# Optimization experiments

Measured on AMD Instinct MI355X. Metric: run time of the kernel, lower is better.

## Reference

```python
import jax, jax.numpy as jnp
import numpy as np

N_HEAD, D_MODEL, D_K, D_V = 8, 128, 16, 16
EPS = 1e-5


def entmax15(x):
    # 1.5-entmax along last axis (Peters & Martins 2019, exact sort-based algo)
    x = x * 0.5
    x = x - jnp.max(x, axis=-1, keepdims=True)
    xs = jnp.flip(jnp.sort(x, axis=-1), axis=-1)  # descending
    K = x.shape[-1]
    rho = jnp.arange(1, K + 1, dtype=x.dtype)
    mean = jnp.cumsum(xs, axis=-1) / rho
    mean_sq = jnp.cumsum(xs * xs, axis=-1) / rho
    delta = (1.0 - rho * (mean_sq - mean * mean)) / rho
    tau = mean - jnp.sqrt(jnp.clip(delta, 0.0))
    support = jnp.sum(tau <= xs, axis=-1, keepdims=True)  # support size k*
    tau_star = jnp.take_along_axis(tau, support - 1, axis=-1)
    p = jnp.clip(x - tau_star, 0.0)
    return p * p


def layer_norm(x, gamma, beta):
    mu = jnp.mean(x, axis=-1, keepdims=True)
    var = jnp.mean((x - mu) ** 2, axis=-1, keepdims=True)
    return gamma * (x - mu) * jax.lax.rsqrt(var + EPS) + beta


def setup_inputs() -> dict:
    key = jax.random.key(0)
    ks = jax.random.split(key, 24)
    B, Lq, Lk, D = 4, 1024, 2048, D_MODEL
    s = 0.05
    f = jax.random.normal
    return {
        "q": f(ks[0], (B, Lq, D), jnp.float32),
        "k": f(ks[1], (B, Lk, D), jnp.float32),
        "v": f(ks[2], (B, Lk, D), jnp.float32),
        "v_2": f(ks[3], (B, Lq, D), jnp.float32),
        "W_Q": f(ks[4], (D, N_HEAD * D_K)) * s, "b_Q": f(ks[5], (N_HEAD * D_K,)) * s,
        "W_K": f(ks[6], (D, N_HEAD * D_K)) * s, "b_K": f(ks[7], (N_HEAD * D_K,)) * s,
        "W_V": f(ks[8], (D, N_HEAD * D_V)) * s, "b_V": f(ks[9], (N_HEAD * D_V,)) * s,
        "W_V2": f(ks[10], (D, N_HEAD * D_V)) * s, "b_V2": f(ks[11], (N_HEAD * D_V,)) * s,
        "W_O": f(ks[12], (N_HEAD * D_V, D)) * s, "b_O": f(ks[13], (D,)) * s,
        "W_O2": f(ks[14], (N_HEAD * D_V, D)) * s, "b_O2": f(ks[15], (D,)) * s,
        "W_R": f(ks[16], (D, D)) * s,
        "W_R2": f(ks[17], (D, D)) * s,
        "gamma": jnp.ones((D,), jnp.float32),
        "beta": jnp.zeros((D,), jnp.float32),
    }


def reference(q, k, v, v_2, W_Q, b_Q, W_K, b_K, W_V, b_V, W_V2, b_V2,
              W_O, b_O, W_O2, b_O2, W_R, W_R2, gamma, beta):
    B, Lq, _ = q.shape
    Lk = k.shape[1]
    Q = (q @ W_Q + b_Q).reshape(B, Lq, N_HEAD, D_K)
    Kh = (k @ W_K + b_K).reshape(B, Lk, N_HEAD, D_K)
    V = (v @ W_V + b_V).reshape(B, Lk, N_HEAD, D_V)
    V2 = (v_2 @ W_V2 + b_V2).reshape(B, Lq, N_HEAD, D_V)
    # scores: [B, H, Lq, Lk]
    scores = jnp.einsum('bqhd,bkhd->bhqk', Q, Kh) / np.float32(np.sqrt(D_K))
    A = entmax15(scores)                              # normalize over Lk
    A2 = entmax15(jnp.swapaxes(scores, -2, -1))       # normalize over Lq
    out = jnp.einsum('bhqk,bkhd->bqhd', A, V).reshape(B, Lq, N_HEAD * D_V)
    out2 = jnp.einsum('bhkq,bqhd->bkhd', A2, V2).reshape(B, Lk, N_HEAD * D_V)
    # dropout is identity in eval mode; both branches use the SAME layer_norm params (as in source)
    out = jax.nn.relu(layer_norm(out @ W_O + b_O + q @ W_R, gamma, beta))
    out2 = jax.nn.relu(layer_norm(out2 @ W_O2 + b_O2 + k @ W_R2, gamma, beta))
    return (out, out2, A, A2)
```

## Files before the change

kernel.cpp:

```cpp
#include <hip/hip_runtime.h>

__device__ __forceinline__ float dpp_scan_add(float x)
{
  x += __int_as_float(__builtin_amdgcn_update_dpp(0, __float_as_int(x), 0x111, 0xf, 0xf, true));
  x += __int_as_float(__builtin_amdgcn_update_dpp(0, __float_as_int(x), 0x112, 0xf, 0xf, true));
  x += __int_as_float(__builtin_amdgcn_update_dpp(0, __float_as_int(x), 0x114, 0xf, 0xf, true));
  x += __int_as_float(__builtin_amdgcn_update_dpp(0, __float_as_int(x), 0x118, 0xf, 0xf, true));
  x += __int_as_float(__builtin_amdgcn_update_dpp(0, __float_as_int(x), 0x142, 0xa, 0xf, true));
  x += __int_as_float(__builtin_amdgcn_update_dpp(0, __float_as_int(x), 0x143, 0xc, 0xf, true));
  return x;
}
__device__ __forceinline__ int dpp_scan_add_i(int x)
{
  x += __builtin_amdgcn_update_dpp(0, x, 0x111, 0xf, 0xf, true);
  x += __builtin_amdgcn_update_dpp(0, x, 0x112, 0xf, 0xf, true);
  x += __builtin_amdgcn_update_dpp(0, x, 0x114, 0xf, 0xf, true);
  x += __builtin_amdgcn_update_dpp(0, x, 0x118, 0xf, 0xf, true);
  x += __builtin_amdgcn_update_dpp(0, x, 0x142, 0xa, 0xf, true);
  x += __builtin_amdgcn_update_dpp(0, x, 0x143, 0xc, 0xf, true);
  return x;
}
__device__ __forceinline__ float wave_bcast63(float x)
{
  return __int_as_float(__builtin_amdgcn_readlane(__float_as_int(x), 63));
}
__device__ __forceinline__ float wave_sum(float x)
{
  return wave_bcast63(dpp_scan_add(x));
}
__device__ __forceinline__ float wave_max(float x)
{
  x = fmaxf(x, __int_as_float(__builtin_amdgcn_update_dpp(__float_as_int(x), __float_as_int(x), 0x111, 0xf, 0xf, false)));
  x = fmaxf(x, __int_as_float(__builtin_amdgcn_update_dpp(__float_as_int(x), __float_as_int(x), 0x112, 0xf, 0xf, false)));
  x = fmaxf(x, __int_as_float(__builtin_amdgcn_update_dpp(__float_as_int(x), __float_as_int(x), 0x114, 0xf, 0xf, false)));
  x = fmaxf(x, __int_as_float(__builtin_amdgcn_update_dpp(__float_as_int(x), __float_as_int(x), 0x118, 0xf, 0xf, false)));
  x = fmaxf(x, __int_as_float(__builtin_amdgcn_update_dpp(__float_as_int(x), __float_as_int(x), 0x142, 0xa, 0xf, false)));
  x = fmaxf(x, __int_as_float(__builtin_amdgcn_update_dpp(__float_as_int(x), __float_as_int(x), 0x143, 0xc, 0xf, false)));
  return wave_bcast63(x);
}

__global__ __launch_bounds__(128) void proj_all_kernel(
    const float* __restrict__ q, const float* __restrict__ k,
    const float* __restrict__ v, const float* __restrict__ v2,
    const float* __restrict__ W_Q, const float* __restrict__ b_Q,
    const float* __restrict__ W_K, const float* __restrict__ b_K,
    const float* __restrict__ W_V, const float* __restrict__ b_V,
    const float* __restrict__ W_V2, const float* __restrict__ b_V2,
    float* __restrict__ Qp, float* __restrict__ Kp,
    float* __restrict__ Vp, float* __restrict__ V2p)
{
  __shared__ float xs[4][128];
  int blk = blockIdx.x;
  const float *X, *W, *B; float* Y; int L, chunked, rb;
  if (blk < 1024)      { X = q;  W = W_Q;  B = b_Q;  Y = Qp;  L = 1024; chunked = 1; rb = blk; }
  else if (blk < 3072) { X = k;  W = W_K;  B = b_K;  Y = Kp;  L = 2048; chunked = 1; rb = blk - 1024; }
  else if (blk < 5120) { X = v;  W = W_V;  B = b_V;  Y = Vp;  L = 2048; chunked = 0; rb = blk - 3072; }
  else                 { X = v2; W = W_V2; B = b_V2; Y = V2p; L = 1024; chunked = 0; rb = blk - 5120; }
  rb *= 4;
  int c = threadIdx.x;
#pragma unroll
  for (int i = 0; i < 4; ++i)
    xs[i][c] = X[(size_t)(rb + i) * 128 + c];
  __syncthreads();
  float b = B[c];
  float a0 = b, a1 = b, a2 = b, a3 = b;
#pragma unroll 8
  for (int d = 0; d < 128; ++d) {
    float w = W[d * 128 + c];
    a0 = fmaf(xs[0][d], w, a0);
    a1 = fmaf(xs[1][d], w, a1);
    a2 = fmaf(xs[2][d], w, a2);
    a3 = fmaf(xs[3][d], w, a3);
  }
  int h = c >> 4, dd = c & 15;
  float av[4] = { a0, a1, a2, a3 };
#pragma unroll
  for (int i = 0; i < 4; ++i) {
    int row = rb + i;
    int bb = row / L;
    int l  = row - bb * L;
    if (chunked)
      Y[(((size_t)(bb * 8 + h) * 4 + (dd >> 2)) * L + l) * 4 + (dd & 3)] = av[i];
    else
      Y[((size_t)(bb * 8 + h) * L + l) * 16 + dd] = av[i];
  }
}

static __device__ __forceinline__ float hstep(float f, float s1, float cnt)
{
  float arg = fmaf(-cnt, f, s1 * s1);
  return (arg > 0.f) ? f / (s1 + sqrtf(arg)) : f / (2.f * s1);
}

template<int LROW, int LCOL>
__global__ __launch_bounds__(256) void attn_kernel(
    const float* __restrict__ RowM, const float* __restrict__ ColM,
    const float* __restrict__ ValM, float* __restrict__ Aout,
    float* __restrict__ OutWs)
{
  constexpr int J     = LCOL / 64;
  constexpr int CAP   = 512;
  constexpr int SLOTS = CAP / 64;
  constexpr float Z   = 1.0f;
  __shared__ float          sval[4][CAP];
  __shared__ unsigned short sidx[4][CAP];

  int ws   = threadIdx.x >> 6;
  int wid  = blockIdx.x * 4 + ws;
  int lane = threadIdx.x & 63;
  int bh   = wid / LROW;
  int r    = wid - bh * LROW;
  int bb   = bh >> 3, h = bh & 7;

  float qf[16];
  { const float* qb = RowM + (size_t)bh * LROW * 16;
#pragma unroll
    for (int d = 0; d < 16; ++d)
      qf[d] = qb[((size_t)(d >> 2) * LROW + r) * 4 + (d & 3)] * 0.125f;
  }

  float x[J];
  const float4* Cb = (const float4*)(ColM + (size_t)bh * LCOL * 16);
#pragma unroll
  for (int j = 0; j < J; ++j) {
    int kk = lane + 64 * j;
    float4 k0 = Cb[0 * LCOL + kk];
    float  s  = qf[0] * k0.x;
    s = fmaf(qf[1], k0.y, s); s = fmaf(qf[2], k0.z, s); s = fmaf(qf[3], k0.w, s);
    float4 k1 = Cb[1 * LCOL + kk];
    s = fmaf(qf[4], k1.x, s); s = fmaf(qf[5], k1.y, s);
    s = fmaf(qf[6], k1.z, s); s = fmaf(qf[7], k1.w, s);
    float4 k2 = Cb[2 * LCOL + kk];
    s = fmaf(qf[8], k2.x, s); s = fmaf(qf[9], k2.y, s);
    s = fmaf(qf[10], k2.z, s); s = fmaf(qf[11], k2.w, s);
    float4 k3 = Cb[3 * LCOL + kk];
    s = fmaf(qf[12], k3.x, s); s = fmaf(qf[13], k3.y, s);
    s = fmaf(qf[14], k3.z, s); s = fmaf(qf[15], k3.w, s);
    x[j] = s;
  }

  float ml = -1e30f, sl = 0.f, ql = 0.f;
#pragma unroll
  for (int j = 0; j < J; ++j) {
    ml = fmaxf(ml, x[j]);
    sl += x[j];
    ql = fmaf(x[j], x[j], ql);
  }
  float m  = wave_max(ml);
  float sr = wave_sum(sl);
  float qr = wave_sum(ql);
  float mu  = sr * (1.f / (float)LCOL);
  float sig = sqrtf(fmaxf(qr * (1.f / (float)LCOL) - mu * mu, 0.f));
  float theta = fmaxf(fmaf(Z, sig, mu), m - 1.0f);

  float* arow = Aout + ((size_t)bh * LROW + r) * LCOL;
  const float* Vb = ValM + (size_t)bh * LCOL * 16;
  float* op = OutWs + ((size_t)bb * LROW + r) * 128 + h * 16;

  int c = 0;
#pragma unroll
  for (int j = 0; j < J; ++j) c += (x[j] > theta) ? 1 : 0;
  int pre  = dpp_scan_add_i(c);
  int base = pre - c;
  int tot  = __builtin_amdgcn_readlane(pre, 63);

  if (tot >= 1 && tot <= CAP) {
    int w = 0;
#pragma unroll
    for (int j = 0; j < J; ++j) {
      if (x[j] > theta) {
        sval[ws][base + w] = x[j];
        sidx[ws][base + w] = (unsigned short)(lane + 64 * j);
        ++w;
      }
    }
    __threadfence_block();

    float sv[SLOTS];
    int   iv[SLOTS];
#pragma unroll
    for (int u = 0; u < SLOTS; ++u) {
      int i2 = lane + u * 64;
      bool ok = i2 < tot;
      sv[u] = ok ? sval[ws][i2] : -1e30f;
      iv[u] = ok ? (int)sidx[ws][i2] : 0;
    }

    float tau = theta;
    bool valid = true;
    for (int it = 0; it < 24; ++it) {
      float s1l = 0.f, s2l = 0.f, cml = 0.f;
#pragma unroll
      for (int u = 0; u < SLOTS; ++u) {
        float t = sv[u] - tau, r0 = fmaxf(t, 0.f);
        s1l += r0; s2l = fmaf(r0, r0, s2l);
        cml += (t > 0.f) ? 1.f : 0.f;
      }
      float s1 = dpp_scan_add(s1l);
      float s2 = dpp_scan_add(s2l);
      float cm = dpp_scan_add(cml);
      s1 = wave_bcast63(s1); s2 = wave_bcast63(s2); cm = wave_bcast63(cm);
      float f = s2 - 1.0f;
      if (it == 0 && f < -1e-6f) { valid = false; break; }
      if (f > 1e-6f && s1 > 1e-12f) tau += hstep(f, s1, cm);
      else break;
    }

    if (valid) {
#pragma unroll
      for (int j = 0; j < J; ++j) {
        int kk = lane + 64 * j;
        float t = fmaxf(x[j] - tau, 0.f);
        arow[kk] = t * t;
      }

      float acc[16];
#pragma unroll
      for (int d = 0; d < 16; ++d) acc[d] = 0.f;
#pragma unroll
      for (int u = 0; u < SLOTS; ++u) {
        if (sv[u] > tau) {
          float t = sv[u] - tau;
          float p = t * t;
          const float4* vp = (const float4*)(Vb + (size_t)iv[u] * 16);
          float4 v0 = vp[0], v1 = vp[1], v2 = vp[2], v3 = vp[3];
          acc[0]  = fmaf(p, v0.x, acc[0]);  acc[1]  = fmaf(p, v0.y, acc[1]);
          acc[2]  = fmaf(p, v0.z, acc[2]);  acc[3]  = fmaf(p, v0.w, acc[3]);
          acc[4]  = fmaf(p, v1.x, acc[4]);  acc[5]  = fmaf(p, v1.y, acc[5]);
          acc[6]  = fmaf(p, v1.z, acc[6]);  acc[7]  = fmaf(p, v1.w, acc[7]);
          acc[8]  = fmaf(p, v2.x, acc[8]);  acc[9]  = fmaf(p, v2.y, acc[9]);
          acc[10] = fmaf(p, v2.z, acc[10]); acc[11] = fmaf(p, v2.w, acc[11]);
          acc[12] = fmaf(p, v3.x, acc[12]); acc[13] = fmaf(p, v3.y, acc[13]);
          acc[14] = fmaf(p, v3.z, acc[14]); acc[15] = fmaf(p, v3.w, acc[15]);
        }
      }
      float vv = 0.f;
#pragma unroll
      for (int d = 0; d < 16; ++d) {
        float tt = wave_bcast63(dpp_scan_add(acc[d]));
        vv = (lane == d) ? tt : vv;
      }
      if (lane < 16) op[lane] = vv;
      return;
    }
  }

  float tau = m - 1.0f;
  bool done = false;
  for (int it = 0; it < 24; ++it) {
    float a1l = 0.f, a2l = 0.f, acl = 0.f;
#pragma unroll
    for (int j = 0; j < J; ++j) {
      float t = x[j] - tau, r0 = fmaxf(t, 0.f);
      a1l += r0; a2l = fmaf(r0, r0, a2l);
      acl += (t > 0.f) ? 1.f : 0.f;
    }
    float a1 = wave_sum(a1l);
    float a2 = wave_sum(a2l);
    float ac = wave_sum(acl);
    float f = a2 - 1.0f;
    bool g = !done && (f > 1e-6f) && (a1 > 1e-12f);
    if (g) tau += hstep(f, a1, ac); else done = true;
    if (done) break;
  }

  float acc[16];
#pragma unroll
  for (int d = 0; d < 16; ++d) acc[d] = 0.f;
#pragma unroll
  for (int j = 0; j < J; ++j) {
    int kk = lane + 64 * j;
    float t = fmaxf(x[j] - tau, 0.f), p = t * t;
    arow[kk] = p;
    const float4* vp = (const float4*)(Vb + (size_t)kk * 16);
    float4 v0 = vp[0], v1 = vp[1], v2 = vp[2], v3 = vp[3];
    acc[0]  = fmaf(p, v0.x, acc[0]);  acc[1]  = fmaf(p, v0.y, acc[1]);
    acc[2]  = fmaf(p, v0.z, acc[2]);  acc[3]  = fmaf(p, v0.w, acc[3]);
    acc[4]  = fmaf(p, v1.x, acc[4]);  acc[5]  = fmaf(p, v1.y, acc[5]);
    acc[6]  = fmaf(p, v1.z, acc[6]);  acc[7]  = fmaf(p, v1.w, acc[7]);
    acc[8]  = fmaf(p, v2.x, acc[8]);  acc[9]  = fmaf(p, v2.y, acc[9]);
    acc[10] = fmaf(p, v2.z, acc[10]); acc[11] = fmaf(p, v2.w, acc[11]);
    acc[12] = fmaf(p, v3.x, acc[12]); acc[13] = fmaf(p, v3.y, acc[13]);
    acc[14] = fmaf(p, v3.z, acc[14]); acc[15] = fmaf(p, v3.w, acc[15]);
  }
  float vv = 0.f;
#pragma unroll
  for (int d = 0; d < 16; ++d) {
    float tt = wave_bcast63(dpp_scan_add(acc[d]));
    vv = (lane == d) ? tt : vv;
  }
  if (lane < 16) op[lane] = vv;
}

__global__ __launch_bounds__(128) void combine_ln_kernel(
    const float* __restrict__ X1, const float* __restrict__ X2,
    const float* __restrict__ W1, const float* __restrict__ W2,
    const float* __restrict__ bias, const float* __restrict__ gamma,
    const float* __restrict__ beta, float* __restrict__ O)
{
  __shared__ float x1s[4][128], x2s[4][128];
  __shared__ float red[2][8];
  int rb = blockIdx.x * 4;
  int c  = threadIdx.x;
#pragma unroll
  for (int i = 0; i < 4; ++i) {
    x1s[i][c] = X1[(size_t)(rb + i) * 128 + c];
    x2s[i][c] = X2[(size_t)(rb + i) * 128 + c];
  }
  __syncthreads();
  float b = bias[c];
  float a0 = b, a1 = b, a2 = b, a3 = b;
#pragma unroll 8
  for (int d = 0; d < 128; ++d) {
    float w1 = W1[d * 128 + c];
    float w2 = W2[d * 128 + c];
    a0 = fmaf(x1s[0][d], w1, fmaf(x2s[0][d], w2, a0));
    a1 = fmaf(x1s[1][d], w1, fmaf(x2s[1][d], w2, a1));
    a2 = fmaf(x1s[2][d], w1, fmaf(x2s[2][d], w2, a2));
    a3 = fmaf(x1s[3][d], w1, fmaf(x2s[3][d], w2, a3));
  }
  float s0 = wave_bcast63(dpp_scan_add(a0));
  float q0 = wave_bcast63(dpp_scan_add(a0 * a0));
  float s1 = wave_bcast63(dpp_scan_add(a1));
  float q1 = wave_bcast63(dpp_scan_add(a1 * a1));
  float s2 = wave_bcast63(dpp_scan_add(a2));
  float q2 = wave_bcast63(dpp_scan_add(a2 * a2));
  float s3 = wave_bcast63(dpp_scan_add(a3));
  float q3 = wave_bcast63(dpp_scan_add(a3 * a3));
  int wv = c >> 6;
  if ((c & 63) == 0) {
    red[wv][0] = s0; red[wv][1] = q0; red[wv][2] = s1; red[wv][3] = q1;
    red[wv][4] = s2; red[wv][5] = q2; red[wv][6] = s3; red[wv][7] = q3;
  }
  __syncthreads();
  float S0 = red[0][0] + red[1][0], Q0 = red[0][1] + red[1][1];
  float S1 = red[0][2] + red[1][2], Q1 = red[0][3] + red[1][3];
  float S2 = red[0][4] + red[1][4], Q2 = red[0][5] + red[1][5];
  float S3 = red[0][6] + red[1][6], Q3 = red[0][7] + red[1][7];
  float g = gamma[c], be = beta[c];
  float mu, var, rs;
  mu = S0 * (1.f / 128.f); var = fmaxf(Q0 * (1.f / 128.f) - mu * mu, 0.f);
  rs = rsqrtf(var + 1e-5f);
  O[(size_t)(rb + 0) * 128 + c] = fmaxf(fmaf((a0 - mu) * rs, g, be), 0.f);
  mu = S1 * (1.f / 128.f); var = fmaxf(Q1 * (1.f / 128.f) - mu * mu, 0.f);
  rs = rsqrtf(var + 1e-5f);
  O[(size_t)(rb + 1) * 128 + c] = fmaxf(fmaf((a1 - mu) * rs, g, be), 0.f);
  mu = S2 * (1.f / 128.f); var = fmaxf(Q2 * (1.f / 128.f) - mu * mu, 0.f);
  rs = rsqrtf(var + 1e-5f);
  O[(size_t)(rb + 2) * 128 + c] = fmaxf(fmaf((a2 - mu) * rs, g, be), 0.f);
  mu = S3 * (1.f / 128.f); var = fmaxf(Q3 * (1.f / 128.f) - mu * mu, 0.f);
  rs = rsqrtf(var + 1e-5f);
  O[(size_t)(rb + 3) * 128 + c] = fmaxf(fmaf((a3 - mu) * rs, g, be), 0.f);
}

extern "C"
__attribute__((visibility("default"), used))
void kernel_launch(void* const* d_in, const int* in_sizes, int n_in,
                   void* d_out, int out_size, void* d_ws, size_t ws_size,
                   hipStream_t stream)
{
  (void)in_sizes; (void)n_in; (void)out_size; (void)ws_size;
  const float* q     = (const float*)d_in[0];
  const float* k     = (const float*)d_in[1];
  const float* v     = (const float*)d_in[2];
  const float* v2    = (const float*)d_in[3];
  const float* W_Q   = (const float*)d_in[4];
  const float* b_Q   = (const float*)d_in[5];
  const float* W_K   = (const float*)d_in[6];
  const float* b_K   = (const float*)d_in[7];
  const float* W_V   = (const float*)d_in[8];
  const float* b_V   = (const float*)d_in[9];
  const float* W_V2  = (const float*)d_in[10];
  const float* b_V2  = (const float*)d_in[11];
  const float* W_O   = (const float*)d_in[12];
  const float* b_O   = (const float*)d_in[13];
  const float* W_O2  = (const float*)d_in[14];
  const float* b_O2  = (const float*)d_in[15];
  const float* W_R   = (const float*)d_in[16];
  const float* W_R2  = (const float*)d_in[17];
  const float* gamma = (const float*)d_in[18];
  const float* beta  = (const float*)d_in[19];

  char* ws = (char*)d_ws;
  const size_t MB = 1u << 20;
  float* Qp    = (float*)(ws + 0);
  float* Kp    = (float*)(ws + 2 * MB);
  float* Vp    = (float*)(ws + 6 * MB);
  float* V2p   = (float*)(ws + 10 * MB);
  float* outm1 = (float*)(ws + 12 * MB);
  float* outm2 = (float*)(ws + 14 * MB);

  float* out1  = (float*)d_out;
  float* out2  = out1 + (size_t)524288;
  float* Aout  = out1 + (size_t)1572864;
  float* A2out = out1 + (size_t)68681728;

  proj_all_kernel<<<6144, 128, 0, stream>>>(
      q, k, v, v2, W_Q, b_Q, W_K, b_K, W_V, b_V, W_V2, b_V2,
      Qp, Kp, Vp, V2p);

  attn_kernel<1024, 2048><<<8192,  256, 0, stream>>>(Qp, Kp, Vp,  Aout,  outm1);
  attn_kernel<2048, 1024><<<16384, 256, 0, stream>>>(Kp, Qp, V2p, A2out, outm2);

  combine_ln_kernel<<<1024, 128, 0, stream>>>(outm1, q, W_O,  W_R,  b_O,
                                              gamma, beta, out1);
  combine_ln_kernel<<<2048, 128, 0, stream>>>(outm2, k, W_O2, W_R2, b_O2,
                                              gamma, beta, out2);
}
```

Measured before the change: 1.096 ms.

## Process two attention rows per wavefront, sharing key loads and splitting sparse phase by half-wave

Each wavefront now computes scores for two query rows at once, so every key float4 loaded from global memory feeds two dot products. The sparse entmax refinement and the value accumulation are split so each 32-lane half-wave handles one row, using a 32-lane DPP scan and a loop over the compacted candidates instead of fixed slots. Grid sizes are halved to match. The change raises register pressure from doubled score arrays. The half-waves also become coupled: the dense fallback now runs for both rows whenever either row fails the candidate test.

```diff
diff --git a/kernel.cpp b/kernel.cpp
--- a/kernel.cpp
+++ b/kernel.cpp
@@ -20,14 +20,21 @@
   x += __builtin_amdgcn_update_dpp(0, x, 0x143, 0xc, 0xf, true);
   return x;
 }
-__device__ __forceinline__ float wave_bcast63(float x)
-{
-  return __int_as_float(__builtin_amdgcn_readlane(__float_as_int(x), 63));
-}
-__device__ __forceinline__ float wave_sum(float x)
-{
-  return wave_bcast63(dpp_scan_add(x));
-}
+__device__ __forceinline__ float dpp_hscan_add(float x)
+{
+  x += __int_as_float(__builtin_amdgcn_update_dpp(0, __float_as_int(x), 0x111, 0xf, 0xf, true));
+  x += __int_as_float(__builtin_amdgcn_update_dpp(0, __float_as_int(x), 0x112, 0xf, 0xf, true));
+  x += __int_as_float(__builtin_amdgcn_update_dpp(0, __float_as_int(x), 0x114, 0xf, 0xf, true));
+  x += __int_as_float(__builtin_amdgcn_update_dpp(0, __float_as_int(x), 0x118, 0xf, 0xf, true));
+  x += __int_as_float(__builtin_amdgcn_update_dpp(0, __float_as_int(x), 0x142, 0xa, 0xf, true));
+  return x;
+}
+__device__ __forceinline__ float rlf(float x, int l)
+{
+  return __int_as_float(__builtin_amdgcn_readlane(__float_as_int(x), l));
+}
+__device__ __forceinline__ float wave_bcast63(float x) { return rlf(x, 63); }
+__device__ __forceinline__ float wave_sum(float x) { return wave_bcast63(dpp_scan_add(x)); }
 __device__ __forceinline__ float wave_max(float x)
 {
   x = fmaxf(x, __int_as_float(__builtin_amdgcn_update_dpp(__float_as_int(x), __float_as_int(x), 0x111, 0xf, 0xf, false)));
@@ -98,131 +105,157 @@
     const float* __restrict__ ValM, float* __restrict__ Aout,
     float* __restrict__ OutWs)
 {
-  constexpr int J     = LCOL / 64;
-  constexpr int CAP   = 512;
-  constexpr int SLOTS = CAP / 64;
-  constexpr float Z   = 1.0f;
-  __shared__ float          sval[4][CAP];
-  __shared__ unsigned short sidx[4][CAP];
+  constexpr int J   = LCOL / 64;
+  constexpr int CAP = 512;
+  constexpr float Z = 1.0f;
+  __shared__ float          sval[4][2][CAP];
+  __shared__ unsigned short sidx[4][2][CAP];
 
   int ws   = threadIdx.x >> 6;
-  int wid  = blockIdx.x * 4 + ws;
+  int pid  = blockIdx.x * 4 + ws;
   int lane = threadIdx.x & 63;
-  int bh   = wid / LROW;
-  int r    = wid - bh * LROW;
+  int half   = lane >> 5;
+  int lane31 = lane & 31;
+  int bh   = pid / (LROW / 2);
+  int pr   = pid - bh * (LROW / 2);
+  int row0 = pr * 2;
   int bb   = bh >> 3, h = bh & 7;
 
-  float qf[16];
+  float qf0[16], qf1[16];
   { const float* qb = RowM + (size_t)bh * LROW * 16;
 #pragma unroll
-    for (int d = 0; d < 16; ++d)
-      qf[d] = qb[((size_t)(d >> 2) * LROW + r) * 4 + (d & 3)] * 0.125f;
-  }
-
-  float x[J];
+    for (int d = 0; d < 16; ++d) {
+      qf0[d] = qb[((size_t)(d >> 2) * LROW + row0)     * 4 + (d & 3)] * 0.125f;
+      qf1[d] = qb[((size_t)(d >> 2) * LROW + row0 + 1) * 4 + (d & 3)] * 0.125f;
+    } }
+
+  float x0[J], x1[J];
   const float4* Cb = (const float4*)(ColM + (size_t)bh * LCOL * 16);
 #pragma unroll
   for (int j = 0; j < J; ++j) {
     int kk = lane + 64 * j;
     float4 k0 = Cb[0 * LCOL + kk];
-    float  s  = qf[0] * k0.x;
-    s = fmaf(qf[1], k0.y, s); s = fmaf(qf[2], k0.z, s); s = fmaf(qf[3], k0.w, s);
     float4 k1 = Cb[1 * LCOL + kk];
-    s = fmaf(qf[4], k1.x, s); s = fmaf(qf[5], k1.y, s);
-    s = fmaf(qf[6], k1.z, s); s = fmaf(qf[7], k1.w, s);
     float4 k2 = Cb[2 * LCOL + kk];
-    s = fmaf(qf[8], k2.x, s); s = fmaf(qf[9], k2.y, s);
-    s = fmaf(qf[10], k2.z, s); s = fmaf(qf[11], k2.w, s);
     float4 k3 = Cb[3 * LCOL + kk];
-    s = fmaf(qf[12], k3.x, s); s = fmaf(qf[13], k3.y, s);
-    s = fmaf(qf[14], k3.z, s); s = fmaf(qf[15], k3.w, s);
-    x[j] = s;
-  }
-
-  float ml = -1e30f, sl = 0.f, ql = 0.f;
+    float s0, s1;
+    s0 = qf0[0] * k0.x;                  s1 = qf1[0] * k0.x;
+    s0 = fmaf(qf0[1],  k0.y, s0);        s1 = fmaf(qf1[1],  k0.y, s1);
+    s0 = fmaf(qf0[2],  k0.z, s0);        s1 = fmaf(qf1[2],  k0.z, s1);
+    s0 = fmaf(qf0[3],  k0.w, s0);        s1 = fmaf(qf1[3],  k0.w, s1);
+    s0 = fmaf(qf0[4],  k1.x, s0);        s1 = fmaf(qf1[4],  k1.x, s1);
+    s0 = fmaf(qf0[5],  k1.y, s0);        s1 = fmaf(qf1[5],  k1.y, s1);
+    s0 = fmaf(qf0[6],  k1.z, s0);        s1 = fmaf(qf1[6],  k1.z, s1);
+    s0 = fmaf(qf0[7],  k1.w, s0);        s1 = fmaf(qf1[7],  k1.w, s1);
+    s0 = fmaf(qf0[8],  k2.x, s0);        s1 = fmaf(qf1[8],  k2.x, s1);
+    s0 = fmaf(qf0[9],  k2.y, s0);        s1 = fmaf(qf1[9],  k2.y, s1);
+    s0 = fmaf(qf0[10], k2.z, s0);        s1 = fmaf(qf1[10], k2.z, s1);
+    s0 = fmaf(qf0[11], k2.w, s0);        s1 = fmaf(qf1[11], k2.w, s1);
+    s0 = fmaf(qf0[12], k3.x, s0);        s1 = fmaf(qf1[12], k3.x, s1);
+    s0 = fmaf(qf0[13], k3.y, s0);        s1 = fmaf(qf1[13], k3.y, s1);
+    s0 = fmaf(qf0[14], k3.z, s0);        s1 = fmaf(qf1[14], k3.z, s1);
+    s0 = fmaf(qf0[15], k3.w, s0);        s1 = fmaf(qf1[15], k3.w, s1);
+    x0[j] = s0; x1[j] = s1;
+  }
+
+  float m0l = -1e30f, s0l = 0.f, q0l = 0.f;
+  float m1l = -1e30f, s1l = 0.f, q1l = 0.f;
 #pragma unroll
   for (int j = 0; j < J; ++j) {
-    ml = fmaxf(ml, x[j]);
-    sl += x[j];
-    ql = fmaf(x[j], x[j], ql);
-  }
-  float m  = wave_max(ml);
-  float sr = wave_sum(sl);
-  float qr = wave_sum(ql);
-  float mu  = sr * (1.f / (float)LCOL);
-  float sig = sqrtf(fmaxf(qr * (1.f / (float)LCOL) - mu * mu, 0.f));
-  float theta = fmaxf(fmaf(Z, sig, mu), m - 1.0f);
-
-  float* arow = Aout + ((size_t)bh * LROW + r) * LCOL;
+    m0l = fmaxf(m0l, x0[j]); s0l += x0[j]; q0l = fmaf(x0[j], x0[j], q0l);
+    m1l = fmaxf(m1l, x1[j]); s1l += x1[j]; q1l = fmaf(x1[j], x1[j], q1l);
+  }
+  float m0 = wave_max(m0l), sr0 = wave_sum(s0l), qr0 = wave_sum(q0l);
+  float m1 = wave_max(m1l), sr1 = wave_sum(s1l), qr1 = wave_sum(q1l);
+  float mu0 = sr0 * (1.f / (float)LCOL);
+  float mu1 = sr1 * (1.f / (float)LCOL);
+  float sg0 = sqrtf(fmaxf(qr0 * (1.f / (float)LCOL) - mu0 * mu0, 0.f));
+  float sg1 = sqrtf(fmaxf(qr1 * (1.f / (float)LCOL) - mu1 * mu1, 0.f));
+  float th0 = fmaxf(fmaf(Z, sg0, mu0), m0 - 1.0f);
+  float th1 = fmaxf(fmaf(Z, sg1, mu1), m1 - 1.0f);
+
+  float* arow = Aout + ((size_t)bh * LROW + row0) * LCOL;
   const float* Vb = ValM + (size_t)bh * LCOL * 16;
-  float* op = OutWs + ((size_t)bb * LROW + r) * 128 + h * 16;
-
-  int c = 0;
-#pragma unroll
-  for (int j = 0; j < J; ++j) c += (x[j] > theta) ? 1 : 0;
-  int pre  = dpp_scan_add_i(c);
-  int base = pre - c;
-  int tot  = __builtin_amdgcn_readlane(pre, 63);
-
-  if (tot >= 1 && tot <= CAP) {
-    int w = 0;
+  float* op = OutWs + ((size_t)bb * LROW + row0) * 128 + h * 16;
+
+  int c0 = 0, c1 = 0;
+#pragma unroll
+  for (int j = 0; j < J; ++j) {
+    c0 += (x0[j] > th0) ? 1 : 0;
+    c1 += (x1[j] > th1) ? 1 : 0;
+  }
+  int pre0 = dpp_scan_add_i(c0);
+  int pre1 = dpp_scan_add_i(c1);
+  int base0 = pre0 - c0, base1 = pre1 - c1;
+  int tot0 = __builtin_amdgcn_readlane(pre0, 63);
+  int tot1 = __builtin_amdgcn_readlane(pre1, 63);
+
+  if (tot0 >= 1 && tot0 <= CAP && tot1 >= 1 && tot1 <= CAP) {
+    int w0 = 0, w1 = 0;
 #pragma unroll
     for (int j = 0; j < J; ++j) {
-      if (x[j] > theta) {
-        sval[ws][base + w] = x[j];
-        sidx[ws][base + w] = (unsigned short)(lane + 64 * j);
-        ++w;
+      if (x0[j] > th0) {
+        sval[ws][0][base0 + w0] = x0[j];
+        sidx[ws][0][base0 + w0] = (unsigned short)(lane + 64 * j);
+        ++w0;
+      }
+      if (x1[j] > th1) {
+        sval[ws][1][base1 + w1] = x1[j];
+        sidx[ws][1][base1 + w1] = (unsigned short)(lane + 64 * j);
+        ++w1;
       }
     }
     __threadfence_block();
 
-    float sv[SLOTS];
-    int   iv[SLOTS];
-#pragma unroll
-    for (int u = 0; u < SLOTS; ++u) {
-      int i2 = lane + u * 64;
-      bool ok = i2 < tot;
-      sv[u] = ok ? sval[ws][i2] : -1e30f;
-      iv[u] = ok ? (int)sidx[ws][i2] : 0;
-    }
-
-    float tau = theta;
-    bool valid = true;
+    const float* svp = &sval[ws][half][0];
+    int   tot_my = half ? tot1 : tot0;
+    float tau_my = half ? th1  : th0;
+    bool invalid = false, done = false;
     for (int it = 0; it < 24; ++it) {
-      float s1l = 0.f, s2l = 0.f, cml = 0.f;
-#pragma unroll
-      for (int u = 0; u < SLOTS; ++u) {
-        float t = sv[u] - tau, r0 = fmaxf(t, 0.f);
-        s1l += r0; s2l = fmaf(r0, r0, s2l);
-        cml += (t > 0.f) ? 1.f : 0.f;
-      }
-      float s1 = dpp_scan_add(s1l);
-      float s2 = dpp_scan_add(s2l);
-      float cm = dpp_scan_add(cml);
-      s1 = wave_bcast63(s1); s2 = wave_bcast63(s2); cm = wave_bcast63(cm);
+      float a1 = 0.f, a2 = 0.f, cm = 0.f;
+      for (int i = lane31; i < tot_my; i += 32) {
+        float t = svp[i] - tau_my, r0 = fmaxf(t, 0.f);
+        a1 += r0; a2 = fmaf(r0, r0, a2); cm += (t > 0.f) ? 1.f : 0.f;
+      }
+      float a1s = dpp_hscan_add(a1);
+      float a2s = dpp_hscan_add(a2);
+      float cms = dpp_hscan_add(cm);
+      float s1 = half ? rlf(a1s, 63) : rlf(a1s, 31);
+      float s2 = half ? rlf(a2s, 63) : rlf(a2s, 31);
+      float cc = half ? rlf(cms, 63) : rlf(cms, 31);
       float f = s2 - 1.0f;
-      if (it == 0 && f < -1e-6f) { valid = false; break; }
-      if (f > 1e-6f && s1 > 1e-12f) tau += hstep(f, s1, cm);
-      else break;
-    }
-
-    if (valid) {
+      if (it == 0 && f < -1e-6f) { invalid = true; done = true; }
+      else if (!done) {
+        if (f > 1e-6f && s1 > 1e-12f) tau_my += hstep(f, s1, cc);
+        else done = true;
+      }
+      if (__ballot(done) == ~0ull) break;
+    }
+    bool inv0 = __builtin_amdgcn_readlane((int)invalid, 0)  != 0;
+    bool inv1 = __builtin_amdgcn_readlane((int)invalid, 32) != 0;
+
+    if (!inv0 && !inv1) {
+      float tau0 = rlf(tau_my, 0);
+      float tau1 = rlf(tau_my, 32);
 #pragma unroll
       for (int j = 0; j < J; ++j) {
         int kk = lane + 64 * j;
-        float t = fmaxf(x[j] - tau, 0.f);
-        arow[kk] = t * t;
-      }
-
+        float t0 = fmaxf(x0[j] - tau0, 0.f);
+        float t1 = fmaxf(x1[j] - tau1, 0.f);
+        arow[kk]        = t0 * t0;
+        arow[LCOL + kk] = t1 * t1;
+      }
+
+      const unsigned short* sip = &sidx[ws][half][0];
       float acc[16];
 #pragma unroll
       for (int d = 0; d < 16; ++d) acc[d] = 0.f;
-#pragma unroll
-      for (int u = 0; u < SLOTS; ++u) {
-        if (sv[u] > tau) {
-          float t = sv[u] - tau;
+      for (int i = lane31; i < tot_my; i += 32) {
+        float t = svp[i] - tau_my;
+        if (t > 0.f) {
           float p = t * t;
-          const float4* vp = (const float4*)(Vb + (size_t)iv[u] * 16);
+          int kk = sip[i];
+          const float4* vp = (const float4*)(Vb + (size_t)kk * 16);
           float4 v0 = vp[0], v1 = vp[1], v2 = vp[2], v3 = vp[3];
           acc[0]  = fmaf(p, v0.x, acc[0]);  acc[1]  = fmaf(p, v0.y, acc[1]);
           acc[2]  = fmaf(p, v0.z, acc[2]);  acc[3]  = fmaf(p, v0.w, acc[3]);
@@ -237,59 +270,64 @@
       float vv = 0.f;
 #pragma unroll
       for (int d = 0; d < 16; ++d) {
-        float tt = wave_bcast63(dpp_scan_add(acc[d]));
-        vv = (lane == d) ? tt : vv;
-      }
-      if (lane < 16) op[lane] = vv;
+        float sc = dpp_hscan_add(acc[d]);
+        float td = half ? rlf(sc, 63) : rlf(sc, 31);
+        vv = (lane31 == d) ? td : vv;
+      }
+      if (lane31 < 16) op[half * 128 + lane31] = vv;
       return;
     }
   }
 
-  float tau = m - 1.0f;
-  bool done = false;
-  for (int it = 0; it < 24; ++it) {
-    float a1l = 0.f, a2l = 0.f, acl = 0.f;
+#pragma unroll
+  for (int pass = 0; pass < 2; ++pass) {
+    float tau = (pass ? m1 : m0) - 1.0f;
+    bool done = false;
+    for (int it = 0; it < 24; ++it) {
+      float a1l = 0.f, a2l = 0.f, acl = 0.f;
+#pragma unroll
+      for (int j = 0; j < J; ++j) {
+        float xv = pass ? x1[j] : x0[j];
+        float t = xv - tau, r0 = fmaxf(t, 0.f);
+        a1l += r0; a2l = fmaf(r0, r0, a2l);
+        acl += (t > 0.f) ? 1.f : 0.f;
+      }
+      float a1 = wave_sum(a1l);
+      float a2 = wave_sum(a2l);
+      float ac = wave_sum(acl);
+      float f = a2 - 1.0f;
+      bool g = !done && (f > 1e-6f) && (a1 > 1e-12f);
+      if (g) tau += hstep(f, a1, ac); else done = true;
+      if (done) break;
+    }
+    float acc[16];
+#pragma unroll
+    for (int d = 0; d < 16; ++d) acc[d] = 0.f;
 #pragma unroll
     for (int j = 0; j < J; ++j) {
-      float t = x[j] - tau, r0 = fmaxf(t, 0.f);
-      a1l += r0; a2l = fmaf(r0, r0, a2l);
-      acl += (t > 0.f) ? 1.f : 0.f;
-    }
-    float a1 = wave_sum(a1l);
-    float a2 = wave_sum(a2l);
-    float ac = wave_sum(acl);
-    float f = a2 - 1.0f;
-    bool g = !done && (f > 1e-6f) && (a1 > 1e-12f);
-    if (g) tau += hstep(f, a1, ac); else done = true;
-    if (done) break;
-  }
-
-  float acc[16];
-#pragma unroll
-  for (int d = 0; d < 16; ++d) acc[d] = 0.f;
-#pragma unroll
-  for (int j = 0; j < J; ++j) {
-    int kk = lane + 64 * j;
-    float t = fmaxf(x[j] - tau, 0.f), p = t * t;
-    arow[kk] = p;
-    const float4* vp = (const float4*)(Vb + (size_t)kk * 16);
-    float4 v0 = vp[0], v1 = vp[1], v2 = vp[2], v3 = vp[3];
-    acc[0]  = fmaf(p, v0.x, acc[0]);  acc[1]  = fmaf(p, v0.y, acc[1]);
-    acc[2]  = fmaf(p, v0.z, acc[2]);  acc[3]  = fmaf(p, v0.w, acc[3]);
-    acc[4]  = fmaf(p, v1.x, acc[4]);  acc[5]  = fmaf(p, v1.y, acc[5]);
-    acc[6]  = fmaf(p, v1.z, acc[6]);  acc[7]  = fmaf(p, v1.w, acc[7]);
-    acc[8]  = fmaf(p, v2.x, acc[8]);  acc[9]  = fmaf(p, v2.y, acc[9]);
-    acc[10] = fmaf(p, v2.z, acc[10]); acc[11] = fmaf(p, v2.w, acc[11]);
-    acc[12] = fmaf(p, v3.x, acc[12]); acc[13] = fmaf(p, v3.y, acc[13]);
-    acc[14] = fmaf(p, v3.z, acc[14]); acc[15] = fmaf(p, v3.w, acc[15]);
-  }
-  float vv = 0.f;
-#pragma unroll
-  for (int d = 0; d < 16; ++d) {
-    float tt = wave_bcast63(dpp_scan_add(acc[d]));
-    vv = (lane == d) ? tt : vv;
-  }
-  if (lane < 16) op[lane] = vv;
+      int kk = lane + 64 * j;
+      float xv = pass ? x1[j] : x0[j];
+      float t = fmaxf(xv - tau, 0.f), p = t * t;
+      arow[(size_t)pass * LCOL + kk] = p;
+      const float4* vp = (const float4*)(Vb + (size_t)kk * 16);
+      float4 v0 = vp[0], v1 = vp[1], v2 = vp[2], v3 = vp[3];
+      acc[0]  = fmaf(p, v0.x, acc[0]);  acc[1]  = fmaf(p, v0.y, acc[1]);
+      acc[2]  = fmaf(p, v0.z, acc[2]);  acc[3]  = fmaf(p, v0.w, acc[3]);
+      acc[4]  = fmaf(p, v1.x, acc[4]);  acc[5]  = fmaf(p, v1.y, acc[5]);
+      acc[6]  = fmaf(p, v1.z, acc[6]);  acc[7]  = fmaf(p, v1.w, acc[7]);
+      acc[8]  = fmaf(p, v2.x, acc[8]);  acc[9]  = fmaf(p, v2.y, acc[9]);
+      acc[10] = fmaf(p, v2.z, acc[10]); acc[11] = fmaf(p, v2.w, acc[11]);
+      acc[12] = fmaf(p, v3.x, acc[12]); acc[13] = fmaf(p, v3.y, acc[13]);
+      acc[14] = fmaf(p, v3.z, acc[14]); acc[15] = fmaf(p, v3.w, acc[15]);
+    }
+    float vv = 0.f;
+#pragma unroll
+    for (int d = 0; d < 16; ++d) {
+      float tt = wave_bcast63(dpp_scan_add(acc[d]));
+      vv = (lane == d) ? tt : vv;
+    }
+    if (lane < 16) op[pass * 128 + lane] = vv;
+  }
 }
 
 __global__ __launch_bounds__(128) void combine_ln_kernel(
@@ -399,8 +437,8 @@
       q, k, v, v2, W_Q, b_Q, W_K, b_K, W_V, b_V, W_V2, b_V2,
       Qp, Kp, Vp, V2p);
 
-  attn_kernel<1024, 2048><<<8192,  256, 0, stream>>>(Qp, Kp, Vp,  Aout,  outm1);
-  attn_kernel<2048, 1024><<<16384, 256, 0, stream>>>(Kp, Qp, V2p, A2out, outm2);
+  attn_kernel<1024, 2048><<<4096, 256, 0, stream>>>(Qp, Kp, Vp,  Aout,  outm1);
+  attn_kernel<2048, 1024><<<8192, 256, 0, stream>>>(Kp, Qp, V2p, A2out, outm2);
 
   combine_ln_kernel<<<1024, 128, 0, stream>>>(outm1, q, W_O,  W_R,  b_O,
                                               gamma, beta, out1);
```

After: 1.093 ms. Within noise of the previous version (-0.3%).
